# Optimization experiments

Measured on AMD Instinct MI355X. Metric: run time of the kernel, lower is better.

The kernel has to match this reference:

```python
import jax, jax.numpy as jnp
import numpy as np

N_NODES = 100_000
N_EDGES = 3_200_000
IN_FEATS = 256
N_HIDDEN = 256
N_CLASSES = 40


def setup_inputs() -> dict:
    key = jax.random.key(0)
    k1, k2, k3, k4, k5, k6 = jax.random.split(key, 6)
    x = jax.random.normal(k1, (N_NODES, IN_FEATS), dtype=jnp.float32)
    edge_index = jax.random.randint(k2, (2, N_EDGES), 0, N_NODES, dtype=jnp.int64)
    edge_vals = jax.random.uniform(k3, (N_EDGES,), dtype=jnp.float32)
    # Glorot-ish scaled weights
    W1 = jax.random.normal(k4, (IN_FEATS, N_HIDDEN), dtype=jnp.float32) / np.sqrt(IN_FEATS)
    W2 = jax.random.normal(k5, (N_HIDDEN, N_HIDDEN), dtype=jnp.float32) / np.sqrt(N_HIDDEN)
    W3 = jax.random.normal(k6, (N_HIDDEN, N_CLASSES), dtype=jnp.float32) / np.sqrt(N_HIDDEN)
    return {"x": x, "edge_index": edge_index, "edge_vals": edge_vals,
            "W1": W1, "W2": W2, "W3": W3}


def _spmm(edge_index, edge_vals, h):
    """Sparse adjacency times dense features: out[dst] += val * h[src]."""
    src = edge_index[0]
    dst = edge_index[1]
    msgs = h[src] * edge_vals[:, None]          # [E, d]
    return jax.ops.segment_sum(msgs, dst, num_segments=h.shape[0])


def reference(x, edge_index, edge_vals, W1, W2, W3):
    # Layer 1: A @ H @ W1, relu
    h = _spmm(edge_index, edge_vals, x) @ W1
    h = jax.nn.relu(h)
    # Layer 2: A @ H @ W2, relu
    h = _spmm(edge_index, edge_vals, h) @ W2
    h = jax.nn.relu(h)
    # Layer 3: A @ H @ W3
    h = _spmm(edge_index, edge_vals, h) @ W3
    # final log_softmax over class dim
    return jax.nn.log_softmax(h, axis=1)
```

## Files before the change

### kernel.cpp

```cpp
#include <hip/hip_runtime.h>
#include <math.h>

#define NN 100000
#define NE 3200000
#define FD 256
#define NC 40
#define BN_BUCK 196

typedef unsigned int u32;
typedef __attribute__((ext_vector_type(8))) short short8;
typedef __attribute__((ext_vector_type(4))) float f32x4;

#define AS1 __attribute__((address_space(1)))
#define AS3 __attribute__((address_space(3)))

static __device__ __forceinline__ float bf2f(unsigned short h) {
    return __builtin_bit_cast(float, ((u32)h) << 16);
}
static __device__ __forceinline__ unsigned short f2bf(float f) {
    u32 u = __builtin_bit_cast(u32, f);
    u += 0x7fffu + ((u >> 16) & 1u);
    return (unsigned short)(u >> 16);
}


__global__ __launch_bounds__(256) void bucket_count(const int* __restrict__ ei_dst, int* __restrict__ gcount) {
    __shared__ int sh[BN_BUCK];
    int t = threadIdx.x;
    if (t < BN_BUCK) sh[t] = 0;
    __syncthreads();
    int i = blockIdx.x * 1024 + t * 4;
    int4 d = *reinterpret_cast<const int4*>(ei_dst + i);
    atomicAdd(&sh[d.x >> 9], 1);
    atomicAdd(&sh[d.y >> 9], 1);
    atomicAdd(&sh[d.z >> 9], 1);
    atomicAdd(&sh[d.w >> 9], 1);
    __syncthreads();
    if (t < BN_BUCK && sh[t]) atomicAdd(&gcount[t], sh[t]);
}

__global__ __launch_bounds__(256) void bucket_scan(const int* __restrict__ gcount,
                                                   int* __restrict__ bucketBase,
                                                   int* __restrict__ bucketFill,
                                                   int* __restrict__ row_ptr) {
    __shared__ int s[256];
    int t = threadIdx.x;
    int v = (t < BN_BUCK) ? gcount[t] : 0;
    s[t] = v;
    __syncthreads();
    for (int d = 1; d < 256; d <<= 1) {
        int x = (t >= d) ? s[t - d] : 0;
        __syncthreads();
        s[t] += x;
        __syncthreads();
    }
    int excl = s[t] - v;
    if (t < BN_BUCK) {
        bucketBase[t] = excl;
        bucketFill[t] = excl;
    }
    if (t == 0) {
        bucketBase[BN_BUCK] = NE;
        row_ptr[NN] = NE;
    }
}

__global__ __launch_bounds__(256) void partition_edges(const int* __restrict__ ei, const float* __restrict__ ev,
                                                       int* __restrict__ bucketFill, int2* __restrict__ ebuf) {
    __shared__ int cnt[BN_BUCK];
    __shared__ int gb[BN_BUCK];
    __shared__ int fill[BN_BUCK];
    int t = threadIdx.x;
    if (t < BN_BUCK) { cnt[t] = 0; fill[t] = 0; }
    __syncthreads();
    int i = blockIdx.x * 1024 + t * 4;
    int4 s4 = *reinterpret_cast<const int4*>(ei + i);
    int4 d4 = *reinterpret_cast<const int4*>(ei + NE + i);
    float4 v4 = *reinterpret_cast<const float4*>(ev + i);
    int b0 = d4.x >> 9, b1 = d4.y >> 9, b2 = d4.z >> 9, b3 = d4.w >> 9;
    atomicAdd(&cnt[b0], 1);
    atomicAdd(&cnt[b1], 1);
    atomicAdd(&cnt[b2], 1);
    atomicAdd(&cnt[b3], 1);
    __syncthreads();
    if (t < BN_BUCK && cnt[t]) gb[t] = atomicAdd(&bucketFill[t], cnt[t]);
    __syncthreads();
    int r;
    r = atomicAdd(&fill[b0], 1); ebuf[gb[b0] + r] = make_int2((s4.x << 9) | (d4.x & 511), __float_as_int(v4.x));
    r = atomicAdd(&fill[b1], 1); ebuf[gb[b1] + r] = make_int2((s4.y << 9) | (d4.y & 511), __float_as_int(v4.y));
    r = atomicAdd(&fill[b2], 1); ebuf[gb[b2] + r] = make_int2((s4.z << 9) | (d4.z & 511), __float_as_int(v4.z));
    r = atomicAdd(&fill[b3], 1); ebuf[gb[b3] + r] = make_int2((s4.w << 9) | (d4.w & 511), __float_as_int(v4.w));
}

__global__ __launch_bounds__(512) void bucket_csr(const int* __restrict__ bucketBase,
                                                  const int2* __restrict__ ebuf,
                                                  int* __restrict__ row_ptr, int2* __restrict__ cp) {
    __shared__ int cnt[512];
    __shared__ int s[512];
    int b = blockIdx.x, t = threadIdx.x;
    int beg = bucketBase[b], end = bucketBase[b + 1];
    cnt[t] = 0;
    __syncthreads();
    for (int e = beg + t; e < end; e += 512)
        atomicAdd(&cnt[ebuf[e].x & 511], 1);
    __syncthreads();
    int c = cnt[t];
    s[t] = c;
    __syncthreads();
    for (int d = 1; d < 512; d <<= 1) {
        int x = (t >= d) ? s[t - d] : 0;
        __syncthreads();
        s[t] += x;
        __syncthreads();
    }
    int excl = s[t] - c;
    int g = b * 512 + t;
    if (g < NN) row_ptr[g] = beg + excl;
    __syncthreads();
    cnt[t] = excl;
    __syncthreads();
    for (int e = beg + t; e < end; e += 512) {
        int2 E = ebuf[e];
        int r = atomicAdd(&cnt[E.x & 511], 1);
        cp[beg + r] = make_int2(E.x >> 9, E.y);
    }
}


__global__ __launch_bounds__(256) void prep(const float* __restrict__ x,
                                            const float* __restrict__ W1,
                                            const float* __restrict__ W2,
                                            const float* __restrict__ W3,
                                            u32* __restrict__ Q, float* __restrict__ Sc,
                                            unsigned short* __restrict__ Wt1,
                                            unsigned short* __restrict__ Wt2,
                                            unsigned short* __restrict__ Wt3p) {
    int b = blockIdx.x, t = threadIdx.x;
    if (b < 25000) {
        int wv = t >> 6, l = t & 63;
        int row = b * 4 + wv;
        float4 v = reinterpret_cast<const float4*>(x)[(size_t)row * 64 + l];
        float m = fmaxf(fmaxf(fabsf(v.x), fabsf(v.y)), fmaxf(fabsf(v.z), fabsf(v.w)));
        for (int d = 32; d > 0; d >>= 1) m = fmaxf(m, __shfl_xor(m, d));
        float inv = (m > 0.f) ? 127.f / m : 0.f;
        int q0 = (int)rintf(v.x * inv), q1 = (int)rintf(v.y * inv);
        int q2 = (int)rintf(v.z * inv), q3 = (int)rintf(v.w * inv);
        u32 pk = (u32)(q0 & 255) | ((u32)(q1 & 255) << 8) | ((u32)(q2 & 255) << 16) | ((u32)(q3 & 255) << 24);
        Q[(size_t)row * 64 + l] = pk;
        if (l == 0) Sc[row] = m * (1.f / 127.f);
    } else if (b < 25256) {
        int n = b - 25000;
        Wt1[n * 256 + t] = f2bf(W1[t * 256 + n]);
    } else if (b < 25512) {
        int n = b - 25256;
        Wt2[n * 256 + t] = f2bf(W2[t * 256 + n]);
    } else {
        int n = b - 25512;
        Wt3p[n * 256 + t] = (n < NC) ? f2bf(W3[t * NC + n]) : (unsigned short)0;
    }
}


template <int UNSIGNED>
__global__ __launch_bounds__(256) void spmm_i8(const int* __restrict__ rp,
                                               const int2* __restrict__ cp,
                                               const u32* __restrict__ Q,
                                               const float* __restrict__ Sc,
                                               unsigned short* __restrict__ O) {
    int wv = threadIdx.x >> 6;
    int l = threadIdx.x & 63;
    int row = blockIdx.x * 4 + wv;
    if (row >= NN) return;
    int beg = __builtin_amdgcn_readfirstlane(rp[row]);
    int end = __builtin_amdgcn_readfirstlane(rp[row + 1]);
    float a0 = 0.f, a1 = 0.f, a2 = 0.f, a3 = 0.f;

#define ACC_I8(W, VS)                                                            \
    {                                                                            \
        u32 w_ = (W);                                                            \
        float p0_, p1_, p2_, p3_;                                                \
        if (UNSIGNED) {                                                          \
            p0_ = (float)(w_ & 255u);        p1_ = (float)((w_ >> 8) & 255u);    \
            p2_ = (float)((w_ >> 16) & 255u); p3_ = (float)(w_ >> 24);           \
        } else {                                                                 \
            p0_ = (float)(int)(char)(w_);        p1_ = (float)(int)(char)(w_ >> 8);  \
            p2_ = (float)(int)(char)(w_ >> 16);  p3_ = (float)(int)(char)(w_ >> 24); \
        }                                                                        \
        a0 += (VS) * p0_; a1 += (VS) * p1_; a2 += (VS) * p2_; a3 += (VS) * p3_;  \
    }

    int e = beg;
    int efull = beg + ((end - beg) & ~15);
    if (e < efull) {
        int2 m[16];
        float vs[16];
#pragma unroll
        for (int j = 0; j < 16; ++j) m[j] = cp[e + j];
#pragma unroll
        for (int j = 0; j < 16; ++j) vs[j] = __int_as_float(m[j].y) * Sc[m[j].x];
        e += 16;
        for (; e < efull; e += 16) {
            u32 hv[16];
#pragma unroll
            for (int j = 0; j < 16; ++j) hv[j] = Q[(size_t)m[j].x * 64 + l];
            int2 mn[16];
            float vsn[16];
#pragma unroll
            for (int j = 0; j < 16; ++j) mn[j] = cp[e + j];
#pragma unroll
            for (int j = 0; j < 16; ++j) vsn[j] = __int_as_float(mn[j].y) * Sc[mn[j].x];
#pragma unroll
            for (int j = 0; j < 16; ++j) ACC_I8(hv[j], vs[j]);
#pragma unroll
            for (int j = 0; j < 16; ++j) { m[j] = mn[j]; vs[j] = vsn[j]; }
        }
        {
            u32 hv[16];
#pragma unroll
            for (int j = 0; j < 16; ++j) hv[j] = Q[(size_t)m[j].x * 64 + l];
#pragma unroll
            for (int j = 0; j < 16; ++j) ACC_I8(hv[j], vs[j]);
        }
    }
    if (end - e >= 8) {
        int2 m[8];
        float vs[8];
#pragma unroll
        for (int j = 0; j < 8; ++j) m[j] = cp[e + j];
#pragma unroll
        for (int j = 0; j < 8; ++j) vs[j] = __int_as_float(m[j].y) * Sc[m[j].x];
        u32 hv[8];
#pragma unroll
        for (int j = 0; j < 8; ++j) hv[j] = Q[(size_t)m[j].x * 64 + l];
#pragma unroll
        for (int j = 0; j < 8; ++j) ACC_I8(hv[j], vs[j]);
        e += 8;
    }
    if (end - e >= 4) {
        int2 m[4];
        float vs[4];
#pragma unroll
        for (int j = 0; j < 4; ++j) m[j] = cp[e + j];
#pragma unroll
        for (int j = 0; j < 4; ++j) vs[j] = __int_as_float(m[j].y) * Sc[m[j].x];
        u32 hv[4];
#pragma unroll
        for (int j = 0; j < 4; ++j) hv[j] = Q[(size_t)m[j].x * 64 + l];
#pragma unroll
        for (int j = 0; j < 4; ++j) ACC_I8(hv[j], vs[j]);
        e += 4;
    }
    if (end - e >= 2) {
        int2 m0 = cp[e];
        int2 m1 = cp[e + 1];
        float v0 = __int_as_float(m0.y) * Sc[m0.x];
        float v1 = __int_as_float(m1.y) * Sc[m1.x];
        u32 h0 = Q[(size_t)m0.x * 64 + l];
        u32 h1 = Q[(size_t)m1.x * 64 + l];
        ACC_I8(h0, v0);
        ACC_I8(h1, v1);
        e += 2;
    }
    for (; e < end; ++e) {
        int2 m1 = cp[e];
        float vs1 = __int_as_float(m1.y) * Sc[m1.x];
        u32 hv = Q[(size_t)m1.x * 64 + l];
        ACC_I8(hv, vs1);
    }
#undef ACC_I8
    ushort4 o;
    o.x = f2bf(a0); o.y = f2bf(a1); o.z = f2bf(a2); o.w = f2bf(a3);
    reinterpret_cast<ushort4*>(O)[(size_t)row * 64 + l] = o;
}

#define BM 128
#define BKK 64


__global__ __launch_bounds__(256) void gemm1_quant(const unsigned short* __restrict__ A,
                                                   const unsigned short* __restrict__ Wt,
                                                   unsigned char* __restrict__ Q8b,
                                                   float* __restrict__ Sc, int M) {
    __shared__ unsigned short As[BM * BKK];
    __shared__ unsigned short Bs[BM * BKK];
    __shared__ unsigned rmax[BM];
    int tid = threadIdx.x;
    int l = tid & 63;
    int w = tid >> 6;
    int wm = w >> 1, wn = w & 1;
    int bm = blockIdx.x * BM;
    if (tid < BM) rmax[tid] = 0u;

    f32x4 acc[4][4];
    u32 p0[4][4][2];

    for (int bh = 0; bh < 2; ++bh) {
        int bn = bh * 128;
#pragma unroll
        for (int m = 0; m < 4; ++m)
#pragma unroll
            for (int n = 0; n < 4; ++n)
                acc[m][n] = (f32x4){0.f, 0.f, 0.f, 0.f};

        for (int kt = 0; kt < 4; ++kt) {
            int k0 = kt * BKK;
#pragma unroll
            for (int i = 0; i < 4; ++i) {
                int e = i * 256 + tid;
                int row = e >> 3;
                int c = e & 7;
                int cs = c ^ (row & 7);
                int ga = min(bm + row, M - 1);
                __builtin_amdgcn_global_load_lds(
                    (const AS1 u32*)(A + (size_t)ga * 256 + k0 + cs * 8),
                    (AS3 u32*)(As + e * 8), 16, 0, 0);
                __builtin_amdgcn_global_load_lds(
                    (const AS1 u32*)(Wt + (size_t)(bn + row) * 256 + k0 + cs * 8),
                    (AS3 u32*)(Bs + e * 8), 16, 0, 0);
            }
            __syncthreads();
#pragma unroll
            for (int h = 0; h < 2; ++h) {
                short8 av[4], bv[4];
#pragma unroll
                for (int m = 0; m < 4; ++m) {
                    int row = wm * 64 + m * 16 + (l & 15);
                    int cs = (h * 4 + (l >> 4)) ^ (row & 7);
                    av[m] = *(const short8*)(As + row * BKK + cs * 8);
                }
#pragma unroll
                for (int n = 0; n < 4; ++n) {
                    int row = wn * 64 + n * 16 + (l & 15);
                    int cs = (h * 4 + (l >> 4)) ^ (row & 7);
                    bv[n] = *(const short8*)(Bs + row * BKK + cs * 8);
                }
#pragma unroll
                for (int m = 0; m < 4; ++m)
#pragma unroll
                    for (int n = 0; n < 4; ++n)
                        acc[m][n] = __builtin_amdgcn_mfma_f32_16x16x32_bf16(av[m], bv[n], acc[m][n], 0, 0, 0);
            }
            __syncthreads();
        }
        if (bh == 0) {
#pragma unroll
            for (int m = 0; m < 4; ++m)
#pragma unroll
                for (int n = 0; n < 4; ++n) {
                    float v0 = fmaxf(acc[m][n][0], 0.f);
                    float v1 = fmaxf(acc[m][n][1], 0.f);
                    float v2 = fmaxf(acc[m][n][2], 0.f);
                    float v3 = fmaxf(acc[m][n][3], 0.f);
                    p0[m][n][0] = (u32)f2bf(v0) | ((u32)f2bf(v1) << 16);
                    p0[m][n][1] = (u32)f2bf(v2) | ((u32)f2bf(v3) << 16);
                }
        }
    }

    float mx[4][4];
#pragma unroll
    for (int m = 0; m < 4; ++m)
#pragma unroll
        for (int r = 0; r < 4; ++r) {
            float v = 0.f;
#pragma unroll
            for (int n = 0; n < 4; ++n) {
                v = fmaxf(v, fmaxf(acc[m][n][r], 0.f));
                u32 pw = p0[m][n][r >> 1];
                unsigned short b = (r & 1) ? (unsigned short)(pw >> 16) : (unsigned short)(pw & 0xffff);
                v = fmaxf(v, bf2f(b));
            }
            v = fmaxf(v, __shfl_xor(v, 1));
            v = fmaxf(v, __shfl_xor(v, 2));
            v = fmaxf(v, __shfl_xor(v, 4));
            v = fmaxf(v, __shfl_xor(v, 8));
            mx[m][r] = v;
        }
    if ((l & 15) == 0) {
#pragma unroll
        for (int m = 0; m < 4; ++m)
#pragma unroll
            for (int r = 0; r < 4; ++r)
                atomicMax(&rmax[wm * 64 + m * 16 + (l >> 4) * 4 + r], __float_as_uint(mx[m][r]));
    }
    __syncthreads();

#pragma unroll
    for (int m = 0; m < 4; ++m)
#pragma unroll
        for (int r = 0; r < 4; ++r) {
            int lr = wm * 64 + m * 16 + (l >> 4) * 4 + r;
            int gr = bm + lr;
            float rm = __uint_as_float(rmax[lr]);
            float inv = (rm > 0.f) ? 255.f / rm : 0.f;
            if (gr < M) {
#pragma unroll
                for (int n = 0; n < 4; ++n) {
                    u32 pw = p0[m][n][r >> 1];
                    unsigned short b = (r & 1) ? (unsigned short)(pw >> 16) : (unsigned short)(pw & 0xffff);
                    int q0v = (int)rintf(bf2f(b) * inv);
                    int q1v = (int)rintf(fmaxf(acc[m][n][r], 0.f) * inv);
                    Q8b[(size_t)gr * 256 + wn * 64 + n * 16 + (l & 15)] = (unsigned char)q0v;
                    Q8b[(size_t)gr * 256 + 128 + wn * 64 + n * 16 + (l & 15)] = (unsigned char)q1v;
                }
                if (wn == 0 && (l & 15) == 0) Sc[gr] = rm * (1.f / 255.f);
            }
        }
}


__global__ __launch_bounds__(256) void gemm_mfma(const unsigned short* __restrict__ A,
                                                 const unsigned short* __restrict__ Wt,
                                                 unsigned short* __restrict__ C, int M, int relu) {
    __shared__ unsigned short As[BM * BKK];
    __shared__ unsigned short Bs[BM * BKK];
    int tid = threadIdx.x;
    int l = tid & 63;
    int w = tid >> 6;
    int wm = w >> 1, wn = w & 1;
    int bm = blockIdx.x * BM;
    int bn = blockIdx.y * BM;

    f32x4 acc[4][4] = {};

    for (int kt = 0; kt < 4; ++kt) {
        int k0 = kt * BKK;
#pragma unroll
        for (int i = 0; i < 4; ++i) {
            int e = i * 256 + tid;
            int row = e >> 3;
            int c = e & 7;
            int cs = c ^ (row & 7);
            int ga = min(bm + row, M - 1);
            __builtin_amdgcn_global_load_lds(
                (const AS1 u32*)(A + (size_t)ga * 256 + k0 + cs * 8),
                (AS3 u32*)(As + e * 8), 16, 0, 0);
            __builtin_amdgcn_global_load_lds(
                (const AS1 u32*)(Wt + (size_t)(bn + row) * 256 + k0 + cs * 8),
                (AS3 u32*)(Bs + e * 8), 16, 0, 0);
        }
        __syncthreads();
#pragma unroll
        for (int h = 0; h < 2; ++h) {
            short8 av[4], bv[4];
#pragma unroll
            for (int m = 0; m < 4; ++m) {
                int row = wm * 64 + m * 16 + (l & 15);
                int cs = (h * 4 + (l >> 4)) ^ (row & 7);
                av[m] = *(const short8*)(As + row * BKK + cs * 8);
            }
#pragma unroll
            for (int n = 0; n < 4; ++n) {
                int row = wn * 64 + n * 16 + (l & 15);
                int cs = (h * 4 + (l >> 4)) ^ (row & 7);
                bv[n] = *(const short8*)(Bs + row * BKK + cs * 8);
            }
#pragma unroll
            for (int m = 0; m < 4; ++m)
#pragma unroll
                for (int n = 0; n < 4; ++n)
                    acc[m][n] = __builtin_amdgcn_mfma_f32_16x16x32_bf16(av[m], bv[n], acc[m][n], 0, 0, 0);
        }
        __syncthreads();
    }

#pragma unroll
    for (int m = 0; m < 4; ++m)
#pragma unroll
        for (int r = 0; r < 4; ++r) {
            int gr = bm + wm * 64 + m * 16 + (l >> 4) * 4 + r;
            if (gr >= M) continue;
#pragma unroll
            for (int n = 0; n < 4; ++n) {
                int gc = bn + wn * 64 + n * 16 + (l & 15);
                float v = acc[m][n][r];
                if (relu) v = fmaxf(v, 0.f);
                C[(size_t)gr * 256 + gc] = f2bf(v);
            }
        }
}


__global__ __launch_bounds__(256) void gemm3_mfma(const unsigned short* __restrict__ H2,
                                                  const unsigned short* __restrict__ Wt3p,
                                                  unsigned short* __restrict__ Lb) {
    int tid = threadIdx.x, l = tid & 63, w = tid >> 6;
    int row0 = blockIdx.x * 64 + w * 16;
    f32x4 acc[3] = {};
    int ra = min(row0 + (l & 15), NN - 1);
    const unsigned short* ap = H2 + (size_t)ra * 256 + (l >> 4) * 8;
#pragma unroll
    for (int kt = 0; kt < 8; ++kt) {
        short8 av = *(const short8*)(ap + kt * 32);
#pragma unroll
        for (int j = 0; j < 3; ++j) {
            const unsigned short* bp = Wt3p + (size_t)(j * 16 + (l & 15)) * 256 + kt * 32 + (l >> 4) * 8;
            short8 bv = *(const short8*)bp;
            acc[j] = __builtin_amdgcn_mfma_f32_16x16x32_bf16(av, bv, acc[j], 0, 0, 0);
        }
    }
#pragma unroll
    for (int j = 0; j < 3; ++j)
#pragma unroll
        for (int r = 0; r < 4; ++r) {
            int gr = row0 + (l >> 4) * 4 + r;
            int gc = j * 16 + (l & 15);
            if (gr < NN && gc < NC) Lb[(size_t)gr * NC + gc] = f2bf(acc[j][r]);
        }
}


__global__ __launch_bounds__(256) void spmm40_lsm(const int* __restrict__ rp,
                                                  const int2* __restrict__ cp,
                                                  const unsigned short* __restrict__ Lb,
                                                  float* __restrict__ out) {
    int wv = threadIdx.x >> 6, l = threadIdx.x & 63;
    int row = blockIdx.x * 4 + wv;
    if (row >= NN) return;
    int beg = __builtin_amdgcn_readfirstlane(rp[row]);
    int end = __builtin_amdgcn_readfirstlane(rp[row + 1]);
    int lc = min(l, NC - 1);
    float acc = 0.f;
    int e = beg;
    int efull = beg + ((end - beg) & ~15);
    if (e < efull) {
        int2 m[16];
#pragma unroll
        for (int j = 0; j < 16; ++j) m[j] = cp[e + j];
        e += 16;
        for (; e < efull; e += 16) {
            unsigned short hv[16];
#pragma unroll
            for (int j = 0; j < 16; ++j) hv[j] = Lb[(size_t)m[j].x * NC + lc];
            int2 mn[16];
#pragma unroll
            for (int j = 0; j < 16; ++j) mn[j] = cp[e + j];
#pragma unroll
            for (int j = 0; j < 16; ++j)
                acc += __int_as_float(m[j].y) * bf2f(hv[j]);
#pragma unroll
            for (int j = 0; j < 16; ++j) m[j] = mn[j];
        }
        {
            unsigned short hv[16];
#pragma unroll
            for (int j = 0; j < 16; ++j) hv[j] = Lb[(size_t)m[j].x * NC + lc];
#pragma unroll
            for (int j = 0; j < 16; ++j)
                acc += __int_as_float(m[j].y) * bf2f(hv[j]);
        }
    }
    if (end - e >= 8) {
        int2 m[8];
#pragma unroll
        for (int j = 0; j < 8; ++j) m[j] = cp[e + j];
        unsigned short hv[8];
#pragma unroll
        for (int j = 0; j < 8; ++j) hv[j] = Lb[(size_t)m[j].x * NC + lc];
#pragma unroll
        for (int j = 0; j < 8; ++j)
            acc += __int_as_float(m[j].y) * bf2f(hv[j]);
        e += 8;
    }
    if (end - e >= 4) {
        int2 m[4];
#pragma unroll
        for (int j = 0; j < 4; ++j) m[j] = cp[e + j];
        unsigned short hv[4];
#pragma unroll
        for (int j = 0; j < 4; ++j) hv[j] = Lb[(size_t)m[j].x * NC + lc];
#pragma unroll
        for (int j = 0; j < 4; ++j)
            acc += __int_as_float(m[j].y) * bf2f(hv[j]);
        e += 4;
    }
    if (end - e >= 2) {
        int2 m0 = cp[e];
        int2 m1 = cp[e + 1];
        unsigned short h0 = Lb[(size_t)m0.x * NC + lc];
        unsigned short h1 = Lb[(size_t)m1.x * NC + lc];
        acc += __int_as_float(m0.y) * bf2f(h0);
        acc += __int_as_float(m1.y) * bf2f(h1);
        e += 2;
    }
    for (; e < end; ++e) {
        int2 m1 = cp[e];
        acc += __int_as_float(m1.y) * bf2f(Lb[(size_t)m1.x * NC + lc]);
    }
    float v = (l < NC) ? acc : -INFINITY;
    float mx = v;
    for (int d = 32; d > 0; d >>= 1) mx = fmaxf(mx, __shfl_xor(mx, d));
    float ex = (l < NC) ? expf(v - mx) : 0.f;
    float ssum = ex;
    for (int d = 32; d > 0; d >>= 1) ssum += __shfl_xor(ssum, d);
    float ls = logf(ssum);
    if (l < NC) out[(size_t)row * NC + l] = v - mx - ls;
}


extern "C" void kernel_launch(void* const* d_in, const int* in_sizes, int n_in,
                              void* d_out, int out_size, void* d_ws, size_t ws_size,
                              hipStream_t stream) {
    const float* x  = (const float*)d_in[0];
    const int*   ei = (const int*)d_in[1];
    const float* ev = (const float*)d_in[2];
    const float* W1 = (const float*)d_in[3];
    const float* W2 = (const float*)d_in[4];
    const float* W3 = (const float*)d_in[5];
    float* out = (float*)d_out;

    char* ws = (char*)d_ws;
    size_t o = 0;
    unsigned short* B0 = (unsigned short*)(ws + o); o += (size_t)NN * FD * 2;
    unsigned short* B1 = (unsigned short*)(ws + o); o += (size_t)NN * FD * 2;
    u32*   Q8          = (u32*)(ws + o);            o += (size_t)NN * FD;
    float* Sc          = (float*)(ws + o);          o += (size_t)NN * 4;
    unsigned short* Lb = (unsigned short*)(ws + o); o += (size_t)NN * NC * 2;
    int2*  cp          = (int2*)(ws + o);           o += (size_t)NE * 8;
    int*   row_ptr     = (int*)(ws + o);            o += 400128;
    int*   gcount      = (int*)(ws + o);            o += 1024;
    int*   bucketBase  = (int*)(ws + o);            o += 1024;
    int*   bucketFill  = (int*)(ws + o);            o += 1024;
    unsigned short* Wt1  = (unsigned short*)(ws + o); o += 256 * 256 * 2;
    unsigned short* Wt2  = (unsigned short*)(ws + o); o += 256 * 256 * 2;
    unsigned short* Wt3p = (unsigned short*)(ws + o); o += 48 * 256 * 2;

    int2* ebuf = (int2*)B1;

    const int EB    = NE / 1024;
    const int RGRID = (NN + 3) / 4;
    const int GXM   = (NN + BM - 1) / BM;
    const int G3    = (NN + 63) / 64;

    hipMemsetAsync(gcount, 0, BN_BUCK * sizeof(int), stream);
    bucket_count<<<EB, 256, 0, stream>>>(ei + NE, gcount);
    bucket_scan<<<1, 256, 0, stream>>>(gcount, bucketBase, bucketFill, row_ptr);
    partition_edges<<<EB, 256, 0, stream>>>(ei, ev, bucketFill, ebuf);
    bucket_csr<<<BN_BUCK, 512, 0, stream>>>(bucketBase, ebuf, row_ptr, cp);

    prep<<<25560, 256, 0, stream>>>(x, W1, W2, W3, Q8, Sc, Wt1, Wt2, Wt3p);

    spmm_i8<0><<<RGRID, 256, 0, stream>>>(row_ptr, cp, Q8, Sc, B1);
    gemm1_quant<<<GXM, 256, 0, stream>>>(B1, Wt1, (unsigned char*)Q8, Sc, NN);

    spmm_i8<1><<<RGRID, 256, 0, stream>>>(row_ptr, cp, Q8, Sc, B1);
    gemm_mfma<<<dim3(GXM, 2), 256, 0, stream>>>(B1, Wt2, B0, NN, 1);

    gemm3_mfma<<<G3, 256, 0, stream>>>(B0, Wt3p, Lb);
    spmm40_lsm<<<RGRID, 256, 0, stream>>>(row_ptr, cp, Lb, out);
}
```

Baseline: 598.9 us.

## Fuse layer-2 GEMM with layer-3 GEMM through shared-memory staging

Merges the W2 GEMM (with ReLU) and the W3 projection into one kernel. Each block computes its 128-row H2 tile in two 128-column halves, stages each half in LDS and immediately multiplies it by the matching slice of W3 into register accumulators. This removes the 51 MB bf16 H2 write and re-read plus one kernel launch. In exchange the A tile is reloaded twice per block, the grid has half as many blocks, and more registers are held live, which may lower occupancy.

```diff
diff --git a/kernel.cpp b/kernel.cpp
--- a/kernel.cpp
+++ b/kernel.cpp
@@ -409,9 +409,10 @@
 }
 
 
-__global__ __launch_bounds__(256) void gemm_mfma(const unsigned short* __restrict__ A,
-                                                 const unsigned short* __restrict__ Wt,
-                                                 unsigned short* __restrict__ C, int M, int relu) {
+__global__ __launch_bounds__(256) void gemm23(const unsigned short* __restrict__ A,
+                                              const unsigned short* __restrict__ Wt2,
+                                              const unsigned short* __restrict__ Wt3p,
+                                              unsigned short* __restrict__ Lb, int M) {
     __shared__ unsigned short As[BM * BKK];
     __shared__ unsigned short Bs[BM * BKK];
     int tid = threadIdx.x;
@@ -419,94 +420,108 @@
     int w = tid >> 6;
     int wm = w >> 1, wn = w & 1;
     int bm = blockIdx.x * BM;
-    int bn = blockIdx.y * BM;
-
-    f32x4 acc[4][4] = {};
-
-    for (int kt = 0; kt < 4; ++kt) {
-        int k0 = kt * BKK;
-#pragma unroll
-        for (int i = 0; i < 4; ++i) {
-            int e = i * 256 + tid;
-            int row = e >> 3;
-            int c = e & 7;
-            int cs = c ^ (row & 7);
-            int ga = min(bm + row, M - 1);
-            __builtin_amdgcn_global_load_lds(
-                (const AS1 u32*)(A + (size_t)ga * 256 + k0 + cs * 8),
-                (AS3 u32*)(As + e * 8), 16, 0, 0);
-            __builtin_amdgcn_global_load_lds(
-                (const AS1 u32*)(Wt + (size_t)(bn + row) * 256 + k0 + cs * 8),
-                (AS3 u32*)(Bs + e * 8), 16, 0, 0);
+
+    f32x4 acc[4][4];
+    f32x4 acc2[2][3] = {};
+
+    for (int bh = 0; bh < 2; ++bh) {
+        int bn = bh * 128;
+#pragma unroll
+        for (int m = 0; m < 4; ++m)
+#pragma unroll
+            for (int n = 0; n < 4; ++n)
+                acc[m][n] = (f32x4){0.f, 0.f, 0.f, 0.f};
+
+        for (int kt = 0; kt < 4; ++kt) {
+            int k0 = kt * BKK;
+#pragma unroll
+            for (int i = 0; i < 4; ++i) {
+                int e = i * 256 + tid;
+                int row = e >> 3;
+                int c = e & 7;
+                int cs = c ^ (row & 7);
+                int ga = min(bm + row, M - 1);
+                __builtin_amdgcn_global_load_lds(
+                    (const AS1 u32*)(A + (size_t)ga * 256 + k0 + cs * 8),
+                    (AS3 u32*)(As + e * 8), 16, 0, 0);
+                __builtin_amdgcn_global_load_lds(
+                    (const AS1 u32*)(Wt2 + (size_t)(bn + row) * 256 + k0 + cs * 8),
+                    (AS3 u32*)(Bs + e * 8), 16, 0, 0);
+            }
+            __syncthreads();
+#pragma unroll
+            for (int h = 0; h < 2; ++h) {
+                short8 av[4], bv[4];
+#pragma unroll
+                for (int m = 0; m < 4; ++m) {
+                    int row = wm * 64 + m * 16 + (l & 15);
+                    int cs = (h * 4 + (l >> 4)) ^ (row & 7);
+                    av[m] = *(const short8*)(As + row * BKK + cs * 8);
+                }
+#pragma unroll
+                for (int n = 0; n < 4; ++n) {
+                    int row = wn * 64 + n * 16 + (l & 15);
+                    int cs = (h * 4 + (l >> 4)) ^ (row & 7);
+                    bv[n] = *(const short8*)(Bs + row * BKK + cs * 8);
+                }
+#pragma unroll
+                for (int m = 0; m < 4; ++m)
+#pragma unroll
+                    for (int n = 0; n < 4; ++n)
+                        acc[m][n] = __builtin_amdgcn_mfma_f32_16x16x32_bf16(av[m], bv[n], acc[m][n], 0, 0, 0);
+            }
+            __syncthreads();
+        }
+
+        {
+            unsigned short* H2s = (wm == 0) ? As : Bs;
+#pragma unroll
+            for (int m = 0; m < 4; ++m)
+#pragma unroll
+                for (int r = 0; r < 4; ++r) {
+                    int lr = m * 16 + (l >> 4) * 4 + r;
+#pragma unroll
+                    for (int n = 0; n < 4; ++n) {
+                        int c = wn * 64 + n * 16 + (l & 15);
+                        int cs = (c >> 3) ^ (lr & 7);
+                        H2s[lr * 128 + cs * 8 + (c & 7)] = f2bf(fmaxf(acc[m][n][r], 0.f));
+                    }
+                }
         }
         __syncthreads();
-#pragma unroll
-        for (int h = 0; h < 2; ++h) {
-            short8 av[4], bv[4];
-#pragma unroll
-            for (int m = 0; m < 4; ++m) {
-                int row = wm * 64 + m * 16 + (l & 15);
-                int cs = (h * 4 + (l >> 4)) ^ (row & 7);
-                av[m] = *(const short8*)(As + row * BKK + cs * 8);
-            }
-#pragma unroll
-            for (int n = 0; n < 4; ++n) {
-                int row = wn * 64 + n * 16 + (l & 15);
-                int cs = (h * 4 + (l >> 4)) ^ (row & 7);
-                bv[n] = *(const short8*)(Bs + row * BKK + cs * 8);
-            }
-#pragma unroll
-            for (int m = 0; m < 4; ++m)
-#pragma unroll
-                for (int n = 0; n < 4; ++n)
-                    acc[m][n] = __builtin_amdgcn_mfma_f32_16x16x32_bf16(av[m], bv[n], acc[m][n], 0, 0, 0);
+
+        {
+            const unsigned short* H2s = (w < 2) ? As : Bs;
+            int lrow = (w & 1) * 32;
+#pragma unroll
+            for (int mm = 0; mm < 2; ++mm) {
+                int lr = lrow + mm * 16 + (l & 15);
+#pragma unroll
+                for (int kc = 0; kc < 4; ++kc) {
+                    int cs = (kc * 4 + (l >> 4)) ^ (lr & 7);
+                    short8 av = *(const short8*)(H2s + lr * 128 + cs * 8);
+#pragma unroll
+                    for (int j3 = 0; j3 < 3; ++j3) {
+                        const unsigned short* bp = Wt3p + (size_t)(j3 * 16 + (l & 15)) * 256 + bh * 128 + kc * 32 + (l >> 4) * 8;
+                        short8 bv = *(const short8*)bp;
+                        acc2[mm][j3] = __builtin_amdgcn_mfma_f32_16x16x32_bf16(av, bv, acc2[mm][j3], 0, 0, 0);
+                    }
+                }
+            }
         }
         __syncthreads();
     }
 
 #pragma unroll
-    for (int m = 0; m < 4; ++m)
-#pragma unroll
-        for (int r = 0; r < 4; ++r) {
-            int gr = bm + wm * 64 + m * 16 + (l >> 4) * 4 + r;
-            if (gr >= M) continue;
-#pragma unroll
-            for (int n = 0; n < 4; ++n) {
-                int gc = bn + wn * 64 + n * 16 + (l & 15);
-                float v = acc[m][n][r];
-                if (relu) v = fmaxf(v, 0.f);
-                C[(size_t)gr * 256 + gc] = f2bf(v);
-            }
-        }
-}
-
-
-__global__ __launch_bounds__(256) void gemm3_mfma(const unsigned short* __restrict__ H2,
-                                                  const unsigned short* __restrict__ Wt3p,
-                                                  unsigned short* __restrict__ Lb) {
-    int tid = threadIdx.x, l = tid & 63, w = tid >> 6;
-    int row0 = blockIdx.x * 64 + w * 16;
-    f32x4 acc[3] = {};
-    int ra = min(row0 + (l & 15), NN - 1);
-    const unsigned short* ap = H2 + (size_t)ra * 256 + (l >> 4) * 8;
-#pragma unroll
-    for (int kt = 0; kt < 8; ++kt) {
-        short8 av = *(const short8*)(ap + kt * 32);
-#pragma unroll
-        for (int j = 0; j < 3; ++j) {
-            const unsigned short* bp = Wt3p + (size_t)(j * 16 + (l & 15)) * 256 + kt * 32 + (l >> 4) * 8;
-            short8 bv = *(const short8*)bp;
-            acc[j] = __builtin_amdgcn_mfma_f32_16x16x32_bf16(av, bv, acc[j], 0, 0, 0);
-        }
-    }
-#pragma unroll
-    for (int j = 0; j < 3; ++j)
-#pragma unroll
-        for (int r = 0; r < 4; ++r) {
-            int gr = row0 + (l >> 4) * 4 + r;
-            int gc = j * 16 + (l & 15);
-            if (gr < NN && gc < NC) Lb[(size_t)gr * NC + gc] = f2bf(acc[j][r]);
-        }
+    for (int mm = 0; mm < 2; ++mm)
+#pragma unroll
+        for (int j3 = 0; j3 < 3; ++j3)
+#pragma unroll
+            for (int r = 0; r < 4; ++r) {
+                int gr = bm + w * 32 + mm * 16 + (l >> 4) * 4 + r;
+                int gc = j3 * 16 + (l & 15);
+                if (gr < M && gc < NC) Lb[(size_t)gr * NC + gc] = f2bf(acc2[mm][j3][r]);
+            }
 }
 
 
@@ -611,7 +626,6 @@
 
     char* ws = (char*)d_ws;
     size_t o = 0;
-    unsigned short* B0 = (unsigned short*)(ws + o); o += (size_t)NN * FD * 2;
     unsigned short* B1 = (unsigned short*)(ws + o); o += (size_t)NN * FD * 2;
     u32*   Q8          = (u32*)(ws + o);            o += (size_t)NN * FD;
     float* Sc          = (float*)(ws + o);          o += (size_t)NN * 4;
@@ -630,7 +644,6 @@
     const int EB    = NE / 1024;
     const int RGRID = (NN + 3) / 4;
     const int GXM   = (NN + BM - 1) / BM;
-    const int G3    = (NN + 63) / 64;
 
     hipMemsetAsync(gcount, 0, BN_BUCK * sizeof(int), stream);
     bucket_count<<<EB, 256, 0, stream>>>(ei + NE, gcount);
@@ -644,8 +657,7 @@
     gemm1_quant<<<GXM, 256, 0, stream>>>(B1, Wt1, (unsigned char*)Q8, Sc, NN);
 
     spmm_i8<1><<<RGRID, 256, 0, stream>>>(row_ptr, cp, Q8, Sc, B1);
-    gemm_mfma<<<dim3(GXM, 2), 256, 0, stream>>>(B1, Wt2, B0, NN, 1);
-
-    gemm3_mfma<<<G3, 256, 0, stream>>>(B0, Wt3p, Lb);
+    gemm23<<<GXM, 256, 0, stream>>>(B1, Wt2, Wt3p, Lb, NN);
+
     spmm40_lsm<<<RGRID, 256, 0, stream>>>(row_ptr, cp, Lb, out);
 }
```

After: 598.0 us. About the same (-0.1%).
